# Kernel optimization log

Measured on AMD Instinct MI355X. Metric: run time of the kernel, lower is better.

## Reference

```python
import jax, jax.numpy as jnp
import numpy as np

B = 8; DIM = 384; H = 8; DH = 48; T = 256; T2 = 64; DEPTH = 4; P = 14; G = 16
SCALE = DIM ** -0.5
BN_INV = 1.0 / float(np.sqrt(1.0 + 1e-5))

def _gelu(x):
    return jax.nn.gelu(x, approximate=False)

def _ln(x, g, b):
    m = x.mean(-1, keepdims=True)
    v = ((x - m) ** 2).mean(-1, keepdims=True)
    return (x - m) / jnp.sqrt(v + 1e-5) * g + b

def _conv(x, w, bi, s, p, groups=1):
    y = jax.lax.conv_general_dilated(x, w, (s, s), [(p, p), (p, p)],
        dimension_numbers=('NCHW', 'OIHW', 'NCHW'), feature_group_count=groups)
    return y + bi[None, :, None, None]

def _gumbel_softmax(logits, key, tau=1.0):
    g = jax.random.gumbel(key, logits.shape, logits.dtype)
    return jax.nn.softmax((logits + g) / tau, axis=-1)

def setup_inputs() -> dict:
    key = jax.random.key(0)
    ks = jax.random.split(key, 20)
    def n(k, shape, s=0.02):
        return jax.random.normal(k, shape, jnp.float32) * s
    D = DEPTH
    return {
        'img': jax.random.normal(ks[0], (B, 3, 224, 224), jnp.float32),
        'adj': jax.random.randint(ks[1], (T, T), 0, 2).astype(jnp.int32),
        'ln_g': jnp.ones((D, DIM), jnp.float32), 'ln_b': jnp.zeros((D, DIM), jnp.float32),
        'gcn_wq': n(ks[2], (D, DH, DH)), 'gcn_wk': n(ks[3], (D, DH, DH)), 'gcn_wv': n(ks[4], (D, DH, DH)),
        'wq': n(ks[5], (D, DIM, DIM)), 'wk': n(ks[6], (D, DIM, DIM)), 'wv': n(ks[7], (D, DIM, DIM)),
        'w_kf': n(ks[8], (D, 2 * DIM, H)), 'w_kf2': n(ks[9], (D, H, T)), 'w_kf3': n(ks[10], (D, H, T2)),
        'sD': jnp.ones((D, H, T), jnp.float32), 'sD2': jnp.ones((D, H, T2), jnp.float32),
        'randmat': n(ks[11], (D, H, H), 1.0),
        'conv1_w': n(ks[12], (DIM, 3, 3, 3), 0.05), 'conv1_b': jnp.zeros((DIM,), jnp.float32),
        'bn_g': jnp.ones((DIM,), jnp.float32), 'bn_b': jnp.zeros((DIM,), jnp.float32),
        'conv2_w': n(ks[13], (DIM, 1, 3, 3), 0.05), 'conv2_b': jnp.zeros((DIM,), jnp.float32),
        'emb_w': n(ks[14], (4 * DIM, DIM)), 'emb_b': jnp.zeros((DIM,), jnp.float32),
        'upool_w': n(ks[15], (DIM, T2)), 'upool_b': jnp.zeros((T2,), jnp.float32),
        'upoolout_w': n(ks[16], (DIM, 1)), 'upoolout_b': jnp.zeros((1,), jnp.float32),
    }

def _forward(img, adj, ln_g, ln_b, gcn_wq, gcn_wk, gcn_wv, wq, wk, wv,
             w_kf, w_kf2, w_kf3, sD, sD2, randmat,
             conv1_w, conv1_b, bn_g, bn_b, conv2_w, conv2_b, emb_w, emb_b,
             upool_w, upool_b, upoolout_w, upoolout_b):
    b = img.shape[0]
    # patchify: (b,3,224,224) -> (b*256, 3, 14, 14)
    x = img.reshape(b, 3, G, P, G, P).transpose(0, 2, 4, 1, 3, 5).reshape(b * G * G, 3, P, P)
    y = _conv(x, conv1_w, conv1_b, 2, 1)                       # (b*256,384,7,7)
    y = y * BN_INV * bn_g[None, :, None, None] + bn_b[None, :, None, None]  # BN eval (mean=0,var=1)
    y = _gelu(y)
    y = _conv(y, conv2_w, conv2_b, 2, 1, groups=DIM)           # depthwise -> (b*256,384,4,4)
    y = y.reshape(b * G * G, DIM, 2, 2, 2, 2).max(axis=(3, 5)) # adaptive max pool -> 2x2
    y = y.reshape(b, G * G, DIM * 4)                           # (b,256, c*p1*p2)
    x = y @ emb_w + emb_b                                      # (b,256,384)
    rep_adj = jnp.broadcast_to(adj.astype(jnp.float32)[None, None], (b, H, T, T))

    def attention(xn, adjbh, i, label):
        t = xn.shape[1]
        x4 = xn.reshape(b, t, H, DH).transpose(0, 2, 1, 3)     # b h t d
        q4 = jnp.einsum('bhts,bhsd->bhtd', adjbh, x4 @ gcn_wq[i])  # GCN: A @ (X W)
        k4 = jnp.einsum('bhts,bhsd->bhtd', adjbh, x4 @ gcn_wk[i])
        q = q4.transpose(0, 2, 1, 3).reshape(b, t, DIM) @ wq[i]
        k = k4.transpose(0, 2, 1, 3).reshape(b, t, DIM) @ wk[i]
        rm0 = _gelu(jnp.concatenate([q, k], -1) @ w_kf[i])     # (b,t,h)
        rm = jnp.einsum('bth,btg->bhg', rm0, rm0)
        if label == 0:
            rmd = jax.nn.sigmoid((rm @ w_kf2[i]) / sD[i])      # (b,h,t)
        else:
            rmd = jax.nn.sigmoid((rm @ w_kf3[i]) / sD2[i])
        qh = q.reshape(b, t, H, DH).transpose(0, 2, 1, 3)
        kh = k.reshape(b, t, H, DH).transpose(0, 2, 1, 3)
        score = jnp.einsum('bhld,bhtd->bhlt', qh, kh) * SCALE
        score = jax.nn.leaky_relu(score)
        score = rmd[:, :, :, None] * score * rmd[:, :, None, :]   # diag_embed(rmd) @ S @ diag_embed(rmd)
        score = jnp.einsum('lh,bhk->blk', randmat[i], score.reshape(b, H, t * t)).reshape(b, H, t, t)
        score = jnp.where(adjbh > 0, score, -1e12)
        attn = jax.nn.softmax(score, axis=-1)
        v4 = jnp.einsum('bhts,bhsd->bhtd', attn, x4 @ gcn_wv[i])  # attn weights as edge weights
        return _gelu(v4.transpose(0, 2, 1, 3).reshape(b, t, DIM) @ wv[i])

    kg = jax.random.key(42)
    for i in range(DEPTH):
        xn = _ln(x, ln_g[i], ln_b[i])
        if i < DEPTH // 2:
            x = attention(xn, rep_adj, i, 0) + x
        else:
            if i == DEPTH // 2:
                tmp = (x @ upool_w + upool_b).transpose(0, 2, 1)       # (b,64,256)
                tmp = _gumbel_softmax(tmp, jax.random.fold_in(kg, i))
                x = tmp @ x                                            # (b,64,384)
                rep_adj = jnp.einsum('bls,bhst->bhlt', tmp, rep_adj)   # C A C^T
                rep_adj = jnp.einsum('bhlt,bmt->bhlm', rep_adj, tmp)
                xn = _ln(x, ln_g[i], ln_b[i])
            x = attention(xn, rep_adj, i, 1) + x

    tmp = (x @ upoolout_w + upoolout_b).transpose(0, 2, 1)             # (b,1,64)
    tmp = _gumbel_softmax(tmp, jax.random.fold_in(kg, 99))
    return tmp @ x                                                     # (b,1,384)

def reference(img, adj, ln_g, ln_b, gcn_wq, gcn_wk, gcn_wv, wq, wk, wv,
              w_kf, w_kf2, w_kf3, sD, sD2, randmat,
              conv1_w, conv1_b, bn_g, bn_b, conv2_w, conv2_b, emb_w, emb_b,
              upool_w, upool_b, upoolout_w, upoolout_b):
    return _forward(img, adj, ln_g, ln_b, gcn_wq, gcn_wk, gcn_wv, wq, wk, wv,
                    w_kf, w_kf2, w_kf3, sD, sD2, randmat,
                    conv1_w, conv1_b, bn_g, bn_b, conv2_w, conv2_b, emb_w, emb_b,
                    upool_w, upool_b, upoolout_w, upoolout_b)
```

## Files before the change

### kernel.cpp

```cpp
#include <hip/hip_runtime.h>
#include <stdint.h>
#include <math.h>

#define NB 8
#define NDIM 384
#define NHD 8
#define DHD 48

__device__ float g_patch[2048 * 1536];
__device__ float g_x[NB * 256 * NDIM];
__device__ float g_xb[NB * 64 * NDIM];
__device__ float g_xq[NB * NHD * 256 * DHD];
__device__ float g_xk[NB * NHD * 256 * DHD];
__device__ float g_xv[NB * NHD * 256 * DHD];
__device__ float g_q4[NB * 256 * NDIM];
__device__ float g_k4[NB * 256 * NDIM];
__device__ float g_q[NB * 256 * NDIM];
__device__ float g_k[NB * 256 * NDIM];
__device__ float g_rm0[NB * 256 * NHD];
__device__ float g_rm[NB * 64];
__device__ float g_rmd[NB * NHD * 256];
__device__ float g_score[NB * NHD * 256 * 256];
__device__ float g_score2[NB * NHD * 256 * 256];
__device__ float g_logits[NB * 256 * 64];
__device__ float g_tmp[NB * 64 * 256];
__device__ float g_e1[NB * 64 * 256];
__device__ float g_adj2[NB * 64 * 64];
__device__ float g_lg2[NB * 64];

__device__ __forceinline__ float* dev_buf(int s) {
  switch (s) {
    case 0: return g_patch;
    case 1: return g_x;
    case 2: return g_q4;
    case 3: return g_k4;
    case 4: return g_q;
    case 5: return g_k;
    case 6: return g_logits;
    default: return nullptr;
  }
}
#define SEL_PATCH 0
#define SEL_X 1
#define SEL_Q4 2
#define SEL_K4 3
#define SEL_Q 4
#define SEL_K 5
#define SEL_LOGITS 6

__device__ __forceinline__ float gelu_f(float x) {
  return 0.5f * x * (1.0f + erff(x * 0.70710678118654752440f));
}

__host__ __device__ inline void threefry2x32(uint32_t k0, uint32_t k1,
                                             uint32_t x0, uint32_t x1,
                                             uint32_t* o0, uint32_t* o1) {
  uint32_t ks2 = k0 ^ k1 ^ 0x1BD11BDAu;
#define TF_R(r) { x0 += x1; x1 = (x1 << (r)) | (x1 >> (32 - (r))); x1 ^= x0; }
  x0 += k0; x1 += k1;
  TF_R(13) TF_R(15) TF_R(26) TF_R(6)
  x0 += k1; x1 += ks2 + 1u;
  TF_R(17) TF_R(29) TF_R(16) TF_R(24)
  x0 += ks2; x1 += k0 + 2u;
  TF_R(13) TF_R(15) TF_R(26) TF_R(6)
  x0 += k0; x1 += k1 + 3u;
  TF_R(17) TF_R(29) TF_R(16) TF_R(24)
  x0 += k1; x1 += ks2 + 4u;
  TF_R(13) TF_R(15) TF_R(26) TF_R(6)
  x0 += ks2; x1 += k0 + 5u;
#undef TF_R
  *o0 = x0; *o1 = x1;
}

__device__ __forceinline__ double gumbel_from(uint32_t k0, uint32_t k1,
                                              uint32_t idx) {
  uint32_t o0, o1;
  threefry2x32(k0, k1, 0u, idx, &o0, &o1);
  uint32_t bits = o0 ^ o1;
  uint32_t ub = (bits >> 9) | 0x3f800000u;
  float f = __uint_as_float(ub) - 1.0f;
  const float tiny = 1.17549435e-38f;
  float u = fmaxf(f + tiny, tiny);
  return -log(-log((double)u));
}

__global__ __launch_bounds__(256) void k_patch(const float* __restrict__ img,
                                               const float* __restrict__ w1, const float* __restrict__ b1,
                                               const float* __restrict__ bng, const float* __restrict__ bnb,
                                               const float* __restrict__ w2, const float* __restrict__ b2) {
  __shared__ float s_in[3 * 16 * 16];
  __shared__ float s_c1[96 * 49];
  __shared__ float s_w1[96 * 27];
  const float BN_INV = (float)0.99999500003749968752;
  int p = blockIdx.x >> 2;
  int chunk = blockIdx.x & 3;
  int obase = chunk * 96;
  int b = p >> 8, g = p & 255, gi = g >> 4, gj = g & 15;
  int tid = threadIdx.x;
  for (int idx = tid; idx < 3 * 256; idx += 256) {
    int c = idx >> 8, r = idx & 255, py = r >> 4, px = r & 15;
    float v = 0.f;
    if (py >= 1 && py <= 14 && px >= 1 && px <= 14)
      v = img[(((size_t)b * 3 + c) * 224 + gi * 14 + py - 1) * 224 + gj * 14 + px - 1];
    s_in[idx] = v;
  }
  const float4* wsrc = (const float4*)(w1 + obase * 27);
  for (int i = tid; i < 96 * 27 / 4; i += 256) ((float4*)s_w1)[i] = wsrc[i];
  __syncthreads();
  int wave = tid >> 6, lane = tid & 63;
  int y = lane / 7, x = lane - y * 7;
  bool act = lane < 49;
  float in[27];
#pragma unroll
  for (int c = 0; c < 3; ++c)
#pragma unroll
    for (int ky = 0; ky < 3; ++ky)
#pragma unroll
      for (int kx = 0; kx < 3; ++kx)
        in[c * 9 + ky * 3 + kx] = act ? s_in[c * 256 + (2 * y + ky) * 16 + (2 * x + kx)] : 0.f;

  for (int ci = 0; ci < 24; ci += 4) {
    int cl0 = wave * 24 + ci;
    int o0 = obase + cl0;
    float a0 = b1[o0], a1 = b1[o0 + 1], a2 = b1[o0 + 2], a3 = b1[o0 + 3];
    const float* wA = s_w1 + cl0 * 27;
#pragma unroll
    for (int j = 0; j < 27; ++j) {
      float ij = in[j];
      a0 += ij * wA[j];
      a1 += ij * wA[27 + j];
      a2 += ij * wA[54 + j];
      a3 += ij * wA[81 + j];
    }
    a0 = a0 * BN_INV * bng[o0] + bnb[o0];
    a1 = a1 * BN_INV * bng[o0 + 1] + bnb[o0 + 1];
    a2 = a2 * BN_INV * bng[o0 + 2] + bnb[o0 + 2];
    a3 = a3 * BN_INV * bng[o0 + 3] + bnb[o0 + 3];
    if (act) {
      s_c1[cl0 * 49 + lane] = gelu_f(a0);
      s_c1[(cl0 + 1) * 49 + lane] = gelu_f(a1);
      s_c1[(cl0 + 2) * 49 + lane] = gelu_f(a2);
      s_c1[(cl0 + 3) * 49 + lane] = gelu_f(a3);
    }
  }
  __syncthreads();
  if (tid < 96) {
    int cl = tid, c = obase + cl;
    float wd[9];
#pragma unroll
    for (int j = 0; j < 9; ++j) wd[j] = w2[c * 9 + j];
    float bb2 = b2[c];
    const float* sc = &s_c1[cl * 49];
    float o2[4][4];
#pragma unroll
    for (int yy = 0; yy < 4; ++yy)
#pragma unroll
      for (int xx = 0; xx < 4; ++xx) {
        float a = bb2;
#pragma unroll
        for (int ky = 0; ky < 3; ++ky) {
          int iy = 2 * yy + ky - 1;
          if (iy < 0 || iy >= 7) continue;
#pragma unroll
          for (int kx = 0; kx < 3; ++kx) {
            int ix = 2 * xx + kx - 1;
            if (ix < 0 || ix >= 7) continue;
            a += sc[iy * 7 + ix] * wd[ky * 3 + kx];
          }
        }
        o2[yy][xx] = a;
      }
    float4 r;
    r.x = fmaxf(fmaxf(o2[0][0], o2[0][1]), fmaxf(o2[1][0], o2[1][1]));
    r.y = fmaxf(fmaxf(o2[0][2], o2[0][3]), fmaxf(o2[1][2], o2[1][3]));
    r.z = fmaxf(fmaxf(o2[2][0], o2[2][1]), fmaxf(o2[3][0], o2[3][1]));
    r.w = fmaxf(fmaxf(o2[2][2], o2[2][3]), fmaxf(o2[3][2], o2[3][3]));
    *(float4*)&g_patch[(size_t)p * 1536 + c * 4] = r;
  }
}

template <int RPB>
__global__ void k_gemm(const float* __restrict__ W, const float* __restrict__ bias,
                       int selA, int selC, int selR,
                       int M, int K, int N, int act) {
  extern __shared__ float sA[];
  const float* A = dev_buf(selA);
  float* C = dev_buf(selC);
  const float* R = (selR >= 0) ? dev_buf(selR) : nullptr;
  int tid = threadIdx.x;
  int bs = blockDim.x;
  int r0 = blockIdx.x * RPB;
  float acc[RPB];
#pragma unroll
  for (int r = 0; r < RPB; ++r) acc[r] = 0.0f;
  const float4 z4 = {0.f, 0.f, 0.f, 0.f};
  for (int k0 = 0; k0 < K; k0 += 384) {
    __syncthreads();
    for (int idx = tid; idx < RPB * 96; idx += bs) {
      int r = idx / 96, q = idx - r * 96;
      int m = r0 + r;
      ((float4*)sA)[idx] = (m < M) ? ((const float4*)(A + (size_t)m * K + k0))[q] : z4;
    }
    __syncthreads();
    const float* Wp = W + (size_t)k0 * N + tid;
    float w0 = Wp[0], w1 = Wp[N], w2 = Wp[2 * (size_t)N], w3 = Wp[3 * (size_t)N];
#pragma unroll 2
    for (int k = 0; k < 384; k += 4) {
      float n0 = 0.f, n1 = 0.f, n2 = 0.f, n3 = 0.f;
      if (k + 4 < 384) {
        const float* Wn = Wp + (size_t)(k + 4) * N;
        n0 = Wn[0]; n1 = Wn[N]; n2 = Wn[2 * (size_t)N]; n3 = Wn[3 * (size_t)N];
      }
#pragma unroll
      for (int r = 0; r < RPB; ++r) {
        float4 a = *(const float4*)&sA[r * 384 + k];
        acc[r] += a.x * w0 + a.y * w1 + a.z * w2 + a.w * w3;
      }
      w0 = n0; w1 = n1; w2 = n2; w3 = n3;
    }
  }
#pragma unroll
  for (int r = 0; r < RPB; ++r) {
    int m = r0 + r;
    if (m >= M) break;
    float v = acc[r];
    if (bias) v += bias[tid];
    if (act == 1) v = gelu_f(v);
    if (R) v += R[(size_t)m * N + tid];
    C[(size_t)m * N + tid] = v;
  }
}

__global__ __launch_bounds__(384) void k_gemm_sk(const float* __restrict__ W, int M, int K, int N) {
  __shared__ float sA[8 * 384];
  int mb = M >> 3;
  int kc = blockIdx.x / mb;
  int rb = blockIdx.x - kc * mb;
  int r0 = rb << 3;
  int k0 = kc * 384;
  int tid = threadIdx.x;
  float acc[8];
#pragma unroll
  for (int r = 0; r < 8; ++r) acc[r] = 0.0f;
  for (int idx = tid; idx < 8 * 96; idx += 384) {
    int r = idx / 96, q = idx - r * 96;
    ((float4*)sA)[idx] = ((const float4*)(g_patch + (size_t)(r0 + r) * K + k0))[q];
  }
  __syncthreads();
  const float* Wp = W + (size_t)k0 * N + tid;
  float w0 = Wp[0], w1 = Wp[N], w2 = Wp[2 * (size_t)N], w3 = Wp[3 * (size_t)N];
#pragma unroll 2
  for (int k = 0; k < 384; k += 4) {
    float n0 = 0.f, n1 = 0.f, n2 = 0.f, n3 = 0.f;
    if (k + 4 < 384) {
      const float* Wn = Wp + (size_t)(k + 4) * N;
      n0 = Wn[0]; n1 = Wn[N]; n2 = Wn[2 * (size_t)N]; n3 = Wn[3 * (size_t)N];
    }
#pragma unroll
    for (int r = 0; r < 8; ++r) {
      float4 a = *(const float4*)&sA[r * 384 + k];
      acc[r] += a.x * w0 + a.y * w1 + a.z * w2 + a.w * w3;
    }
    w0 = n0; w1 = n1; w2 = n2; w3 = n3;
  }
#pragma unroll
  for (int r = 0; r < 8; ++r)
    g_score[((size_t)kc * M + r0 + r) * N + tid] = acc[r];
}

__global__ void k_gemm_skred(const float* __restrict__ bias, int M, int N) {
  int i = blockIdx.x * blockDim.x + threadIdx.x;
  int total = M * N;
  if (i >= total) return;
  size_t stride = (size_t)M * N;
  float v = g_score[i] + g_score[i + stride] + g_score[i + 2 * stride] + g_score[i + 3 * stride];
  g_x[i] = v + bias[i % N];
}

template <int RPB>
__global__ void k_gemmqk(const float* __restrict__ Wq_, const float* __restrict__ Wk_, int M) {
  __shared__ float sA[RPB * 384];
  int half = gridDim.x >> 1;
  bool isK = blockIdx.x >= half;
  int bid = isK ? blockIdx.x - half : blockIdx.x;
  const float* A = isK ? g_k4 : g_q4;
  float* C = isK ? g_k : g_q;
  const float* W = isK ? Wk_ : Wq_;
  const int N = 384;
  int tid = threadIdx.x;
  int r0 = bid * RPB;
  float acc[RPB];
#pragma unroll
  for (int r = 0; r < RPB; ++r) acc[r] = 0.0f;
  for (int idx = tid; idx < RPB * 96; idx += N) {
    int r = idx / 96, q = idx - r * 96;
    ((float4*)sA)[idx] = ((const float4*)(A + (size_t)(r0 + r) * 384))[q];
  }
  __syncthreads();
  const float* Wp = W + tid;
  float w0 = Wp[0], w1 = Wp[N], w2 = Wp[2 * (size_t)N], w3 = Wp[3 * (size_t)N];
#pragma unroll 2
  for (int k = 0; k < 384; k += 4) {
    float n0 = 0.f, n1 = 0.f, n2 = 0.f, n3 = 0.f;
    if (k + 4 < 384) {
      const float* Wn = Wp + (size_t)(k + 4) * N;
      n0 = Wn[0]; n1 = Wn[N]; n2 = Wn[2 * (size_t)N]; n3 = Wn[3 * (size_t)N];
    }
#pragma unroll
    for (int r = 0; r < RPB; ++r) {
      float4 a = *(const float4*)&sA[r * 384 + k];
      acc[r] += a.x * w0 + a.y * w1 + a.z * w2 + a.w * w3;
    }
    w0 = n0; w1 = n1; w2 = n2; w3 = n3;
  }
#pragma unroll
  for (int r = 0; r < RPB; ++r)
    C[(size_t)(r0 + r) * N + tid] = acc[r];
}

__global__ __launch_bounds__(384) void k_lngcn(const float* __restrict__ gg, const float* __restrict__ bb,
                                               const float* __restrict__ Wq, const float* __restrict__ Wk,
                                               const float* __restrict__ Wv, int t) {
  __shared__ float xn[NDIM];
  __shared__ float wred[6];
  int row = blockIdx.x;
  int b = row / t, tt = row - b * t;
  int tid = threadIdx.x;
  int wid = tid >> 6, lane = tid & 63;
  float v = g_x[(size_t)row * NDIM + tid];
  float s = v;
#pragma unroll
  for (int off = 32; off > 0; off >>= 1) s += __shfl_xor(s, off);
  if (lane == 0) wred[wid] = s;
  __syncthreads();
  float tot = wred[0] + wred[1] + wred[2] + wred[3] + wred[4] + wred[5];
  float mean = tot * (1.0f / 384.0f);
  __syncthreads();
  float d = v - mean;
  s = d * d;
#pragma unroll
  for (int off = 32; off > 0; off >>= 1) s += __shfl_xor(s, off);
  if (lane == 0) wred[wid] = s;
  __syncthreads();
  tot = wred[0] + wred[1] + wred[2] + wred[3] + wred[4] + wred[5];
  float var = tot * (1.0f / 384.0f);
  float inv = 1.0f / sqrtf(var + 1e-5f);
  xn[tid] = d * inv * gg[tid] + bb[tid];
  __syncthreads();
  int h = tid / DHD, dd = tid - h * DHD;
  const float* xh = &xn[h * DHD];
  float aq = 0.f, ak = 0.f, av = 0.f;
#pragma unroll 4
  for (int e = 0; e < DHD; ++e) {
    float xv_ = xh[e];
    aq += xv_ * Wq[e * DHD + dd];
    ak += xv_ * Wk[e * DHD + dd];
    av += xv_ * Wv[e * DHD + dd];
  }
  size_t o = ((size_t)(b * NHD + h) * t + tt) * DHD + dd;
  g_xq[o] = aq; g_xk[o] = ak; g_xv[o] = av;
}

__global__ __launch_bounds__(64) void k_adjmm(const int* __restrict__ adji, int use_adj2, int t) {
  __shared__ float arow[4][256];
  int bid = blockIdx.x;
  int nt = t >> 2;
  int lt = bid % nt; int h = (bid / nt) % NHD; int b = bid / (nt * NHD);
  int l0 = lt * 4;
  int tid = threadIdx.x;
  for (int idx = tid; idx < 4 * t; idx += 64) {
    int r = idx / t, s2 = idx - r * t;
    arow[r][s2] = use_adj2 ? g_adj2[((size_t)b * t + l0 + r) * t + s2]
                           : (float)adji[(l0 + r) * 256 + s2];
  }
  __syncthreads();
  if (tid < DHD) {
    const float* xq = g_xq + (size_t)((b * NHD + h) * t) * DHD + tid;
    const float* xk = g_xk + (size_t)((b * NHD + h) * t) * DHD + tid;
    float aq[4] = {0.f, 0.f, 0.f, 0.f}, ak[4] = {0.f, 0.f, 0.f, 0.f};
    for (int s2 = 0; s2 < t; ++s2) {
      float xqv = xq[(size_t)s2 * DHD];
      float xkv = xk[(size_t)s2 * DHD];
#pragma unroll
      for (int r = 0; r < 4; ++r) {
        aq[r] += arow[r][s2] * xqv;
        ak[r] += arow[r][s2] * xkv;
      }
    }
#pragma unroll
    for (int r = 0; r < 4; ++r) {
      size_t o = ((size_t)b * t + l0 + r) * NDIM + h * DHD + tid;
      g_q4[o] = aq[r]; g_k4[o] = ak[r];
    }
  }
}

__global__ __launch_bounds__(64) void k_kf(const float* __restrict__ Wkf) {
  int row = blockIdx.x;
  int tid = threadIdx.x;
  const float* qrow = g_q + (size_t)row * NDIM;
  const float* krow = g_k + (size_t)row * NDIM;
  float accs[8];
#pragma unroll
  for (int j = 0; j < 8; ++j) accs[j] = 0.f;
  for (int m = tid; m < 768; m += 64) {
    float v = (m < 384) ? qrow[m] : krow[m - 384];
    const float* wr = Wkf + (size_t)m * 8;
#pragma unroll
    for (int j = 0; j < 8; ++j) accs[j] += v * wr[j];
  }
#pragma unroll
  for (int j = 0; j < 8; ++j) {
    float a = accs[j];
    for (int off = 32; off > 0; off >>= 1) a += __shfl_xor(a, off);
    if (tid == 0) g_rm0[(size_t)row * 8 + j] = gelu_f(a);
  }
}

__global__ __launch_bounds__(256) void k_rm(int t) {
  __shared__ float red[256];
  int b = blockIdx.x; int tid = threadIdx.x;
  int out = tid & 63, slice = tid >> 6;
  int h = out >> 3, g = out & 7;
  int t4 = t >> 2;
  const float* base = g_rm0 + (size_t)b * t * 8 + (size_t)slice * t4 * 8;
  float acc = 0.f;
  for (int tt = 0; tt < t4; ++tt) acc += base[tt * 8 + h] * base[tt * 8 + g];
  red[slice * 64 + out] = acc;
  __syncthreads();
  if (tid < 64)
    g_rm[b * 64 + tid] = red[tid] + red[64 + tid] + red[128 + tid] + red[192 + tid];
}

__global__ void k_rmd(const float* __restrict__ Wp, const float* __restrict__ sDp, int t) {
  int id = blockIdx.x * blockDim.x + threadIdx.x;
  int total = NB * NHD * t;
  if (id >= total) return;
  int s = id % t; int h = (id / t) % NHD; int b = id / (t * NHD);
  const float* rm = g_rm + b * 64 + h * 8;
  float acc = 0.f;
#pragma unroll
  for (int g = 0; g < 8; ++g) acc += rm[g] * Wp[g * t + s];
  float val = acc / sDp[h * t + s];
  g_rmd[(size_t)(b * NHD + h) * t + s] = 1.0f / (1.0f + expf(-val));
}

__global__ void k_score(float scale, int t) {
  __shared__ float qs[4][DHD];
  __shared__ float rl[4];
  int bid = blockIdx.x;
  int nt = t >> 2;
  int lt = bid % nt; int h = (bid / nt) % NHD; int b = bid / (nt * NHD);
  int l0 = lt * 4;
  int tid = threadIdx.x;
  for (int idx = tid; idx < 4 * DHD; idx += t) {
    int r = idx / DHD, d = idx - r * DHD;
    qs[r][d] = g_q[((size_t)b * t + l0 + r) * NDIM + h * DHD + d];
  }
  if (tid < 4) rl[tid] = g_rmd[(size_t)(b * NHD + h) * t + l0 + tid];
  __syncthreads();
  const float* krow = g_k + ((size_t)b * t + tid) * NDIM + h * DHD;
  float4 kr[12];
#pragma unroll
  for (int j = 0; j < 12; ++j) kr[j] = *(const float4*)&krow[j * 4];
  float rmd_s = g_rmd[(size_t)(b * NHD + h) * t + tid];
#pragma unroll
  for (int r = 0; r < 4; ++r) {
    float acc = 0.f;
#pragma unroll
    for (int j = 0; j < 12; ++j) {
      float4 qq = *(const float4*)&qs[r][j * 4];
      acc += kr[j].x * qq.x + kr[j].y * qq.y + kr[j].z * qq.z + kr[j].w * qq.w;
    }
    float v = acc * scale;
    v = (v >= 0.f) ? v : 0.01f * v;
    v = rl[r] * v * rmd_s;
    g_score[((size_t)(b * NHD + h) * t + l0 + r) * t + tid] = v;
  }
}

__global__ void k_mixsoft(const float* __restrict__ RM, const int* __restrict__ adji,
                          int use_adj2, int t) {
  extern __shared__ float red2[];
  int bid = blockIdx.x;
  int l = bid % t; int h = (bid / t) % NHD; int b = bid / (t * NHD);
  int tid = threadIdx.x;
  float rm[8];
#pragma unroll
  for (int j = 0; j < 8; ++j) rm[j] = RM[h * 8 + j];
  float acc = 0.f;
#pragma unroll
  for (int j = 0; j < 8; ++j)
    acc += rm[j] * g_score[((size_t)(b * NHD + j) * t + l) * t + tid];
  bool m = use_adj2 ? (g_adj2[((size_t)b * t + l) * t + tid] > 0.f)
                    : (adji[l * 256 + tid] > 0);
  float v = m ? acc : -1e12f;
  red2[tid] = v;
  __syncthreads();
  for (int s = t >> 1; s > 0; s >>= 1) { if (tid < s) red2[tid] = fmaxf(red2[tid], red2[tid + s]); __syncthreads(); }
  float mx = red2[0];
  __syncthreads();
  float e = expf(v - mx);
  red2[tid] = e;
  __syncthreads();
  for (int s = t >> 1; s > 0; s >>= 1) { if (tid < s) red2[tid] += red2[tid + s]; __syncthreads(); }
  g_score2[((size_t)(b * NHD + h) * t + l) * t + tid] = e / red2[0];
}

__global__ __launch_bounds__(64) void k_attnv(int t) {
  __shared__ float arow[4][256];
  int bid = blockIdx.x;
  int nt = t >> 2;
  int lt = bid % nt; int h = (bid / nt) % NHD; int b = bid / (nt * NHD);
  int l0 = lt * 4;
  int tid = threadIdx.x;
  for (int idx = tid; idx < 4 * t; idx += 64) {
    int r = idx / t, s2 = idx - r * t;
    arow[r][s2] = g_score2[((size_t)(b * NHD + h) * t + l0 + r) * t + s2];
  }
  __syncthreads();
  if (tid < DHD) {
    const float* xv = g_xv + (size_t)((b * NHD + h) * t) * DHD + tid;
    float acc[4] = {0.f, 0.f, 0.f, 0.f};
    for (int s2 = 0; s2 < t; ++s2) {
      float xvv = xv[(size_t)s2 * DHD];
#pragma unroll
      for (int r = 0; r < 4; ++r) acc[r] += arow[r][s2] * xvv;
    }
#pragma unroll
    for (int r = 0; r < 4; ++r)
      g_q4[((size_t)b * t + l0 + r) * NDIM + h * DHD + tid] = acc[r];
  }
}

__global__ __launch_bounds__(256) void k_gumbel_pool(uint32_t k0, uint32_t k1) {
  __shared__ double red2[256];
  int bj = blockIdx.x;
  int b = bj >> 6, j = bj & 63;
  int tt = threadIdx.x;
  uint32_t n = (uint32_t)bj * 256u + (uint32_t)tt;
  double gum = gumbel_from(k0, k1, n);
  double val = (double)g_logits[((size_t)b * 256 + tt) * 64 + j] + gum;
  red2[tt] = val; __syncthreads();
  for (int s = 128; s > 0; s >>= 1) { if (tt < s) red2[tt] = fmax(red2[tt], red2[tt + s]); __syncthreads(); }
  double mx = red2[0]; __syncthreads();
  double e = exp(val - mx);
  red2[tt] = e; __syncthreads();
  for (int s = 128; s > 0; s >>= 1) { if (tt < s) red2[tt] += red2[tt + s]; __syncthreads(); }
  g_tmp[(size_t)bj * 256 + tt] = (float)(e / red2[0]);
}

__global__ __launch_bounds__(384) void k_poolx() {
  __shared__ float trow[256];
  int bj = blockIdx.x; int b = bj >> 6;
  int tid = threadIdx.x;
  if (tid < 256) trow[tid] = g_tmp[(size_t)bj * 256 + tid];
  __syncthreads();
  float acc = 0.f;
  const float* xb = g_x + (size_t)b * 256 * NDIM + tid;
  for (int tt = 0; tt < 256; ++tt) acc += trow[tt] * xb[(size_t)tt * NDIM];
  g_xb[(size_t)bj * NDIM + tid] = acc;
}

__global__ void k_copyx(int n) {
  int i = blockIdx.x * blockDim.x + threadIdx.x;
  if (i < n) g_x[i] = g_xb[i];
}

__global__ __launch_bounds__(256) void k_pooladj1(const int* __restrict__ adji) {
  __shared__ float trow[256];
  int bl = blockIdx.x;
  int tid = threadIdx.x;
  trow[tid] = g_tmp[(size_t)bl * 256 + tid];
  __syncthreads();
  float acc = 0.f;
  for (int s = 0; s < 256; ++s) acc += trow[s] * (float)adji[s * 256 + tid];
  g_e1[(size_t)bl * 256 + tid] = acc;
}

__global__ __launch_bounds__(64) void k_pooladj2() {
  __shared__ float erow[256];
  int bl = blockIdx.x; int b = bl >> 6;
  int tid = threadIdx.x;
  for (int s = tid; s < 256; s += 64) erow[s] = g_e1[(size_t)bl * 256 + s];
  __syncthreads();
  const float* tm = g_tmp + ((size_t)b * 64 + tid) * 256;
  float acc = 0.f;
  for (int s = 0; s < 256; ++s) acc += erow[s] * tm[s];
  g_adj2[(size_t)bl * 64 + tid] = acc;
}

__global__ __launch_bounds__(64) void k_outlogits(const float* __restrict__ w, const float* __restrict__ bias) {
  int row = blockIdx.x;
  int tid = threadIdx.x;
  const float* x = g_x + (size_t)row * NDIM;
  float acc = 0.f;
  for (int c = tid; c < NDIM; c += 64) acc += x[c] * w[c];
  for (int off = 32; off > 0; off >>= 1) acc += __shfl_xor(acc, off);
  if (tid == 0) g_lg2[row] = acc + bias[0];
}

__global__ __launch_bounds__(384) void k_final(uint32_t k0, uint32_t k1, float* __restrict__ out) {
  __shared__ double sv[64];
  __shared__ double sp[64];
  int b = blockIdx.x;
  int tid = threadIdx.x;
  if (tid < 64) {
    uint32_t n = (uint32_t)(b * 64 + tid);
    sv[tid] = (double)g_lg2[b * 64 + tid] + gumbel_from(k0, k1, n);
  }
  __syncthreads();
  double mx = -1e30;
  for (int i2 = 0; i2 < 64; ++i2) mx = fmax(mx, sv[i2]);
  if (tid < 64) sp[tid] = exp(sv[tid] - mx);
  __syncthreads();
  double sum = 0.;
  for (int i2 = 0; i2 < 64; ++i2) sum += sp[i2];
  float acc = 0.f;
  const float* xb = g_x + (size_t)b * 64 * NDIM + tid;
  for (int tt = 0; tt < 64; ++tt) acc += (float)(sp[tt] / sum) * xb[(size_t)tt * NDIM];
  out[(size_t)b * NDIM + tid] = acc;
}

extern "C" void kernel_launch(void* const* d_in, const int* in_sizes, int n_in,
                              void* d_out, int out_size, void* d_ws, size_t ws_size,
                              hipStream_t stream) {
  const float* img = (const float*)d_in[0];
  const int* adj = (const int*)d_in[1];
  const float* ln_g = (const float*)d_in[2];
  const float* ln_b = (const float*)d_in[3];
  const float* gcn_wq = (const float*)d_in[4];
  const float* gcn_wk = (const float*)d_in[5];
  const float* gcn_wv = (const float*)d_in[6];
  const float* wq = (const float*)d_in[7];
  const float* wk = (const float*)d_in[8];
  const float* wv = (const float*)d_in[9];
  const float* w_kf = (const float*)d_in[10];
  const float* w_kf2 = (const float*)d_in[11];
  const float* w_kf3 = (const float*)d_in[12];
  const float* sD = (const float*)d_in[13];
  const float* sD2 = (const float*)d_in[14];
  const float* randmat = (const float*)d_in[15];
  const float* conv1_w = (const float*)d_in[16];
  const float* conv1_b = (const float*)d_in[17];
  const float* bn_g = (const float*)d_in[18];
  const float* bn_b = (const float*)d_in[19];
  const float* conv2_w = (const float*)d_in[20];
  const float* conv2_b = (const float*)d_in[21];
  const float* emb_w = (const float*)d_in[22];
  const float* emb_b = (const float*)d_in[23];
  const float* upool_w = (const float*)d_in[24];
  const float* upool_b = (const float*)d_in[25];
  const float* upoolout_w = (const float*)d_in[26];
  const float* upoolout_b = (const float*)d_in[27];
  float* out = (float*)d_out;

  uint32_t k2a, k2b, k99a, k99b;
  threefry2x32(0u, 42u, 0u, 2u, &k2a, &k2b);
  threefry2x32(0u, 42u, 0u, 99u, &k99a, &k99b);

  const float SCALE = (float)(1.0 / sqrt(384.0));

  k_patch<<<2048 * 4, 256, 0, stream>>>(img, conv1_w, conv1_b, bn_g, bn_b, conv2_w, conv2_b);
  k_gemm_sk<<<1024, 384, 0, stream>>>(emb_w, 2048, 1536, 384);
  k_gemm_skred<<<(2048 * 384 + 255) / 256, 256, 0, stream>>>(emb_b, 2048, 384);

  auto attention = [&](int i, int t, int label) {
    int rows = NB * t;
    int bht = NB * NHD * t;
    int bht4 = bht / 4;
    int use_adj2 = (t == 64) ? 1 : 0;
    k_lngcn<<<rows, 384, 0, stream>>>(ln_g + i * 384, ln_b + i * 384,
                                      gcn_wq + i * 2304, gcn_wk + i * 2304,
                                      gcn_wv + i * 2304, t);
    k_adjmm<<<bht4, 64, 0, stream>>>(adj, use_adj2, t);
    if (rows == 2048) {
      k_gemmqk<4><<<1024, 384, 0, stream>>>(wq + i * 147456, wk + i * 147456, rows);
    } else {
      k_gemmqk<2><<<512, 384, 0, stream>>>(wq + i * 147456, wk + i * 147456, rows);
    }
    k_kf<<<rows, 64, 0, stream>>>(w_kf + i * 6144);
    k_rm<<<NB, 256, 0, stream>>>(t);
    const float* Wp = label ? (w_kf3 + i * 512) : (w_kf2 + i * 2048);
    const float* sDp = label ? (sD2 + i * 512) : (sD + i * 2048);
    int totr = NB * NHD * t;
    k_rmd<<<(totr + 255) / 256, 256, 0, stream>>>(Wp, sDp, t);
    k_score<<<bht4, t, 0, stream>>>(SCALE, t);
    k_mixsoft<<<bht, t, t * sizeof(float), stream>>>(randmat + i * 64, adj, use_adj2, t);
    k_attnv<<<bht4, 64, 0, stream>>>(t);
    if (rows == 2048) {
      k_gemm<4><<<512, 384, 4 * 384 * sizeof(float), stream>>>(
          wv + i * 147456, nullptr, SEL_Q4, SEL_X, SEL_X, rows, 384, 384, 1);
    } else {
      k_gemm<2><<<256, 384, 2 * 384 * sizeof(float), stream>>>(
          wv + i * 147456, nullptr, SEL_Q4, SEL_X, SEL_X, rows, 384, 384, 1);
    }
  };

  attention(0, 256, 0);
  attention(1, 256, 0);

  k_gemm<2><<<1024, 64, 2 * 384 * sizeof(float), stream>>>(
      upool_w, upool_b, SEL_X, SEL_LOGITS, -1, 2048, 384, 64, 0);
  k_gumbel_pool<<<512, 256, 0, stream>>>(k2a, k2b);
  k_poolx<<<512, 384, 0, stream>>>();
  k_copyx<<<(NB * 64 * NDIM + 255) / 256, 256, 0, stream>>>(NB * 64 * NDIM);
  k_pooladj1<<<512, 256, 0, stream>>>(adj);
  k_pooladj2<<<512, 64, 0, stream>>>();

  attention(2, 64, 1);
  attention(3, 64, 1);

  k_outlogits<<<512, 64, 0, stream>>>(upoolout_w, upoolout_b);
  k_final<<<8, 384, 0, stream>>>(k99a, k99b, out);
}
```

Before: 925.5 us.

## Vectorize patch conv weights, fuse rm/rmd kernels, batch head-mix softmax

Pads the first conv's per-channel weights from 27 to 28 so the inner product can use float4 shared-memory loads, and spreads the depthwise conv stage over 192 threads instead of 96. Merges k_rm and k_rmd into one kernel that keeps the 8x8 head-mix matrix in shared memory, removing a launch and a global round trip. Replaces the per-(b,h,l) mix-softmax with a per-(b,l) kernel that reads all 8 heads once, mixes them in registers and uses wave-shuffle reductions instead of shared-memory tree reductions. In exchange, the fused rm/rmd kernel runs on only 8 blocks, and the mix kernel uses more shared memory per block.

```diff
diff --git a/kernel.cpp b/kernel.cpp
--- a/kernel.cpp
+++ b/kernel.cpp
@@ -18,7 +18,6 @@
 __device__ float g_q[NB * 256 * NDIM];
 __device__ float g_k[NB * 256 * NDIM];
 __device__ float g_rm0[NB * 256 * NHD];
-__device__ float g_rm[NB * 64];
 __device__ float g_rmd[NB * NHD * 256];
 __device__ float g_score[NB * NHD * 256 * 256];
 __device__ float g_score2[NB * NHD * 256 * 256];
@@ -88,9 +87,9 @@
                                                const float* __restrict__ w1, const float* __restrict__ b1,
                                                const float* __restrict__ bng, const float* __restrict__ bnb,
                                                const float* __restrict__ w2, const float* __restrict__ b2) {
-  __shared__ float s_in[3 * 16 * 16];
+  __shared__ float s_in[3 * 256];
   __shared__ float s_c1[96 * 49];
-  __shared__ float s_w1[96 * 27];
+  __shared__ float s_w1[96 * 28];
   const float BN_INV = (float)0.99999500003749968752;
   int p = blockIdx.x >> 2;
   int chunk = blockIdx.x & 3;
@@ -104,13 +103,16 @@
       v = img[(((size_t)b * 3 + c) * 224 + gi * 14 + py - 1) * 224 + gj * 14 + px - 1];
     s_in[idx] = v;
   }
-  const float4* wsrc = (const float4*)(w1 + obase * 27);
-  for (int i = tid; i < 96 * 27 / 4; i += 256) ((float4*)s_w1)[i] = wsrc[i];
+  for (int i = tid; i < 96 * 27; i += 256) {
+    int ch = i / 27, j = i - ch * 27;
+    s_w1[ch * 28 + j] = w1[(size_t)obase * 27 + i];
+  }
+  if (tid < 96) s_w1[tid * 28 + 27] = 0.f;
   __syncthreads();
   int wave = tid >> 6, lane = tid & 63;
   int y = lane / 7, x = lane - y * 7;
   bool act = lane < 49;
-  float in[27];
+  float in[28];
 #pragma unroll
   for (int c = 0; c < 3; ++c)
 #pragma unroll
@@ -118,19 +120,23 @@
 #pragma unroll
       for (int kx = 0; kx < 3; ++kx)
         in[c * 9 + ky * 3 + kx] = act ? s_in[c * 256 + (2 * y + ky) * 16 + (2 * x + kx)] : 0.f;
+  in[27] = 0.f;
 
   for (int ci = 0; ci < 24; ci += 4) {
     int cl0 = wave * 24 + ci;
     int o0 = obase + cl0;
     float a0 = b1[o0], a1 = b1[o0 + 1], a2 = b1[o0 + 2], a3 = b1[o0 + 3];
-    const float* wA = s_w1 + cl0 * 27;
-#pragma unroll
-    for (int j = 0; j < 27; ++j) {
-      float ij = in[j];
-      a0 += ij * wA[j];
-      a1 += ij * wA[27 + j];
-      a2 += ij * wA[54 + j];
-      a3 += ij * wA[81 + j];
+    const float* wA = s_w1 + cl0 * 28;
+#pragma unroll
+    for (int j = 0; j < 28; j += 4) {
+      float4 w0v = *(const float4*)&wA[j];
+      float4 w1v = *(const float4*)&wA[28 + j];
+      float4 w2v = *(const float4*)&wA[56 + j];
+      float4 w3v = *(const float4*)&wA[84 + j];
+      a0 += in[j] * w0v.x + in[j + 1] * w0v.y + in[j + 2] * w0v.z + in[j + 3] * w0v.w;
+      a1 += in[j] * w1v.x + in[j + 1] * w1v.y + in[j + 2] * w1v.z + in[j + 3] * w1v.w;
+      a2 += in[j] * w2v.x + in[j + 1] * w2v.y + in[j + 2] * w2v.z + in[j + 3] * w2v.w;
+      a3 += in[j] * w3v.x + in[j + 1] * w3v.y + in[j + 2] * w3v.z + in[j + 3] * w3v.w;
     }
     a0 = a0 * BN_INV * bng[o0] + bnb[o0];
     a1 = a1 * BN_INV * bng[o0 + 1] + bnb[o0 + 1];
@@ -144,16 +150,17 @@
     }
   }
   __syncthreads();
-  if (tid < 96) {
-    int cl = tid, c = obase + cl;
+  if (tid < 192) {
+    int cl = tid >> 1, half = tid & 1, c = obase + cl;
     float wd[9];
 #pragma unroll
     for (int j = 0; j < 9; ++j) wd[j] = w2[c * 9 + j];
     float bb2 = b2[c];
     const float* sc = &s_c1[cl * 49];
-    float o2[4][4];
-#pragma unroll
-    for (int yy = 0; yy < 4; ++yy)
+    float o2[2][4];
+#pragma unroll
+    for (int y2 = 0; y2 < 2; ++y2) {
+      int yy = half * 2 + y2;
 #pragma unroll
       for (int xx = 0; xx < 4; ++xx) {
         float a = bb2;
@@ -168,14 +175,13 @@
             a += sc[iy * 7 + ix] * wd[ky * 3 + kx];
           }
         }
-        o2[yy][xx] = a;
+        o2[y2][xx] = a;
       }
-    float4 r;
+    }
+    float2 r;
     r.x = fmaxf(fmaxf(o2[0][0], o2[0][1]), fmaxf(o2[1][0], o2[1][1]));
     r.y = fmaxf(fmaxf(o2[0][2], o2[0][3]), fmaxf(o2[1][2], o2[1][3]));
-    r.z = fmaxf(fmaxf(o2[2][0], o2[2][1]), fmaxf(o2[3][0], o2[3][1]));
-    r.w = fmaxf(fmaxf(o2[2][2], o2[2][3]), fmaxf(o2[3][2], o2[3][3]));
-    *(float4*)&g_patch[(size_t)p * 1536 + c * 4] = r;
+    *(float2*)&g_patch[(size_t)p * 1536 + c * 4 + half * 2] = r;
   }
 }
 
@@ -417,8 +423,10 @@
   }
 }
 
-__global__ __launch_bounds__(256) void k_rm(int t) {
+__global__ __launch_bounds__(256) void k_rmrmd(const float* __restrict__ Wp,
+                                               const float* __restrict__ sDp, int t) {
   __shared__ float red[256];
+  __shared__ float rm_s[64];
   int b = blockIdx.x; int tid = threadIdx.x;
   int out = tid & 63, slice = tid >> 6;
   int h = out >> 3, g = out & 7;
@@ -429,20 +437,17 @@
   red[slice * 64 + out] = acc;
   __syncthreads();
   if (tid < 64)
-    g_rm[b * 64 + tid] = red[tid] + red[64 + tid] + red[128 + tid] + red[192 + tid];
-}
-
-__global__ void k_rmd(const float* __restrict__ Wp, const float* __restrict__ sDp, int t) {
-  int id = blockIdx.x * blockDim.x + threadIdx.x;
-  int total = NB * NHD * t;
-  if (id >= total) return;
-  int s = id % t; int h = (id / t) % NHD; int b = id / (t * NHD);
-  const float* rm = g_rm + b * 64 + h * 8;
-  float acc = 0.f;
-#pragma unroll
-  for (int g = 0; g < 8; ++g) acc += rm[g] * Wp[g * t + s];
-  float val = acc / sDp[h * t + s];
-  g_rmd[(size_t)(b * NHD + h) * t + s] = 1.0f / (1.0f + expf(-val));
+    rm_s[tid] = red[tid] + red[64 + tid] + red[128 + tid] + red[192 + tid];
+  __syncthreads();
+  for (int idx = tid; idx < NHD * t; idx += 256) {
+    int s = idx % t; int hh = idx / t;
+    const float* rm = rm_s + hh * 8;
+    float a = 0.f;
+#pragma unroll
+    for (int gg = 0; gg < 8; ++gg) a += rm[gg] * Wp[gg * t + s];
+    float val = a / sDp[hh * t + s];
+    g_rmd[((size_t)(b * NHD + hh)) * t + s] = 1.0f / (1.0f + expf(-val));
+  }
 }
 
 __global__ void k_score(float scale, int t) {
@@ -479,32 +484,58 @@
   }
 }
 
-__global__ void k_mixsoft(const float* __restrict__ RM, const int* __restrict__ adji,
-                          int use_adj2, int t) {
-  extern __shared__ float red2[];
+template <int T>
+__global__ void k_mix8(const float* __restrict__ RM, const int* __restrict__ adji,
+                       int use_adj2) {
+  __shared__ float p[8][T];
+  __shared__ float rmat[64];
   int bid = blockIdx.x;
-  int l = bid % t; int h = (bid / t) % NHD; int b = bid / (t * NHD);
-  int tid = threadIdx.x;
-  float rm[8];
-#pragma unroll
-  for (int j = 0; j < 8; ++j) rm[j] = RM[h * 8 + j];
-  float acc = 0.f;
-#pragma unroll
-  for (int j = 0; j < 8; ++j)
-    acc += rm[j] * g_score[((size_t)(b * NHD + j) * t + l) * t + tid];
-  bool m = use_adj2 ? (g_adj2[((size_t)b * t + l) * t + tid] > 0.f)
-                    : (adji[l * 256 + tid] > 0);
-  float v = m ? acc : -1e12f;
-  red2[tid] = v;
-  __syncthreads();
-  for (int s = t >> 1; s > 0; s >>= 1) { if (tid < s) red2[tid] = fmaxf(red2[tid], red2[tid + s]); __syncthreads(); }
-  float mx = red2[0];
-  __syncthreads();
-  float e = expf(v - mx);
-  red2[tid] = e;
-  __syncthreads();
-  for (int s = t >> 1; s > 0; s >>= 1) { if (tid < s) red2[tid] += red2[tid + s]; __syncthreads(); }
-  g_score2[((size_t)(b * NHD + h) * t + l) * t + tid] = e / red2[0];
+  int l = bid % T, b = bid / T;
+  int tt = threadIdx.x;
+  if (tt < 64) rmat[tt] = RM[tt];
+  __syncthreads();
+  float sv[8];
+#pragma unroll
+  for (int h = 0; h < 8; ++h)
+    sv[h] = g_score[((size_t)(b * NHD + h) * T + l) * T + tt];
+  bool m = use_adj2 ? (g_adj2[((size_t)b * T + l) * T + tt] > 0.f)
+                    : (adji[l * 256 + tt] > 0);
+#pragma unroll
+  for (int g = 0; g < 8; ++g) {
+    float a = 0.f;
+#pragma unroll
+    for (int h = 0; h < 8; ++h) a += rmat[g * 8 + h] * sv[h];
+    p[g][tt] = m ? a : -1e12f;
+  }
+  __syncthreads();
+  int wid = tt >> 6, lane = tt & 63;
+  const int NW = T / 64;
+  const int RPW = 8 / NW;
+  const int EPL = T / 64;
+  for (int rr = 0; rr < RPW; ++rr) {
+    int row = wid * RPW + rr;
+    float mv = -1e30f;
+#pragma unroll
+    for (int e = 0; e < EPL; ++e) mv = fmaxf(mv, p[row][lane + e * 64]);
+#pragma unroll
+    for (int off = 32; off > 0; off >>= 1) mv = fmaxf(mv, __shfl_xor(mv, off));
+    float sum = 0.f;
+#pragma unroll
+    for (int e = 0; e < EPL; ++e) {
+      float ev = expf(p[row][lane + e * 64] - mv);
+      p[row][lane + e * 64] = ev;
+      sum += ev;
+    }
+#pragma unroll
+    for (int off = 32; off > 0; off >>= 1) sum += __shfl_xor(sum, off);
+    float inv = 1.0f / sum;
+#pragma unroll
+    for (int e = 0; e < EPL; ++e) p[row][lane + e * 64] *= inv;
+  }
+  __syncthreads();
+#pragma unroll
+  for (int h = 0; h < 8; ++h)
+    g_score2[((size_t)(b * NHD + h) * T + l) * T + tt] = p[h][tt];
 }
 
 __global__ __launch_bounds__(64) void k_attnv(int t) {
@@ -667,8 +698,7 @@
 
   auto attention = [&](int i, int t, int label) {
     int rows = NB * t;
-    int bht = NB * NHD * t;
-    int bht4 = bht / 4;
+    int bht4 = NB * NHD * t / 4;
     int use_adj2 = (t == 64) ? 1 : 0;
     k_lngcn<<<rows, 384, 0, stream>>>(ln_g + i * 384, ln_b + i * 384,
                                       gcn_wq + i * 2304, gcn_wk + i * 2304,
@@ -680,13 +710,15 @@
       k_gemmqk<2><<<512, 384, 0, stream>>>(wq + i * 147456, wk + i * 147456, rows);
     }
     k_kf<<<rows, 64, 0, stream>>>(w_kf + i * 6144);
-    k_rm<<<NB, 256, 0, stream>>>(t);
     const float* Wp = label ? (w_kf3 + i * 512) : (w_kf2 + i * 2048);
     const float* sDp = label ? (sD2 + i * 512) : (sD + i * 2048);
-    int totr = NB * NHD * t;
-    k_rmd<<<(totr + 255) / 256, 256, 0, stream>>>(Wp, sDp, t);
+    k_rmrmd<<<NB, 256, 0, stream>>>(Wp, sDp, t);
     k_score<<<bht4, t, 0, stream>>>(SCALE, t);
-    k_mixsoft<<<bht, t, t * sizeof(float), stream>>>(randmat + i * 64, adj, use_adj2, t);
+    if (t == 256) {
+      k_mix8<256><<<rows, 256, 0, stream>>>(randmat + i * 64, adj, use_adj2);
+    } else {
+      k_mix8<64><<<rows, 64, 0, stream>>>(randmat + i * 64, adj, use_adj2);
+    }
     k_attnv<<<bht4, 64, 0, stream>>>(t);
     if (rows == 2048) {
       k_gemm<4><<<512, 384, 4 * 384 * sizeof(float), stream>>>(
```

Result: faster. 899.6 us (-2.8%).
